# Kernel optimization log

Measured on AMD Instinct MI355X. Metric: run time of the kernel, lower is better.

## Reference

```python
import jax, jax.numpy as jnp
import numpy as np

OUT_H, OUT_W = 7, 7
SPATIAL_SCALE = 1.0


def setup_inputs() -> dict:
    key = jax.random.key(0)
    B, C, H, W = 4, 256, 64, 64
    N = 128
    features = jax.random.normal(key, (B, C, H, W), dtype=jnp.float32)
    rng = np.random.default_rng(0)
    bidx = rng.integers(0, B, N)
    x1 = rng.integers(0, W - 8, N)
    y1 = rng.integers(0, H - 8, N)
    x2 = np.minimum(x1 + rng.integers(4, 48, N), W - 1)
    y2 = np.minimum(y1 + rng.integers(4, 48, N), H - 1)
    rois = jnp.asarray(np.stack([bidx, x1, y1, x2, y2], axis=1), dtype=jnp.int32)
    return {"features": features, "rois": rois}


def _bin_bounds(n_bins, bin_sz, roi_sz):
    # h_start = int(h*bin_h); h_end = int((h+1)*bin_h); then clamp as in torch code
    bins = jnp.arange(n_bins)
    start = jnp.floor(bins[None, :] * bin_sz[:, None]).astype(jnp.int32)
    end = jnp.floor((bins[None, :] + 1) * bin_sz[:, None]).astype(jnp.int32)
    start = jnp.minimum(start, roi_sz[:, None] - 1)
    end = jnp.minimum(end, roi_sz[:, None])
    return start, end  # [N, n_bins]


def _roi_pool(features, rois):
    B, C, H, W = features.shape
    b = rois[:, 0]
    coords = (rois[:, 1:5].astype(jnp.float32) * SPATIAL_SCALE).astype(jnp.int32)
    x1, y1, x2, y2 = coords[:, 0], coords[:, 1], coords[:, 2], coords[:, 3]
    roi_h = y2 - y1 + 1  # inclusive slice y1:y2+1
    roi_w = x2 - x1 + 1
    bin_h = roi_h.astype(jnp.float32) / OUT_H
    bin_w = roi_w.astype(jnp.float32) / OUT_W

    hs, he = _bin_bounds(OUT_H, bin_h, roi_h)  # [N, OUT_H]
    ws, we = _bin_bounds(OUT_W, bin_w, roi_w)  # [N, OUT_W]
    valid = (he > hs)[:, :, None] & (we > ws)[:, None, :]  # [N, OUT_H, OUT_W]

    yy = jnp.arange(H)
    xx = jnp.arange(W)
    # absolute-coordinate bin masks (factorized along H and W)
    mask_h = (yy[None, None, :] >= (y1[:, None] + hs)[:, :, None]) & (
        yy[None, None, :] < (y1[:, None] + he)[:, :, None])  # [N, OUT_H, H]
    mask_w = (xx[None, None, :] >= (x1[:, None] + ws)[:, :, None]) & (
        xx[None, None, :] < (x1[:, None] + we)[:, :, None])  # [N, OUT_W, W]

    feat = features[b]  # [N, C, H, W] gather per ROI
    NEG = jnp.array(-jnp.inf, features.dtype)
    # reduce H per output row bin (OUT_H is small, fixed)
    rows = [jnp.where(mask_h[:, i, None, :, None], feat, NEG).max(axis=2)
            for i in range(OUT_H)]  # each [N, C, W]
    rowmax = jnp.stack(rows, axis=1)  # [N, OUT_H, C, W]
    cols = [jnp.where(mask_w[:, j, None, None, :], rowmax, NEG).max(axis=3)
            for j in range(OUT_W)]  # each [N, OUT_H, C]
    pooled = jnp.stack(cols, axis=3)  # [N, OUT_H, C, OUT_W]
    pooled = jnp.transpose(pooled, (0, 2, 1, 3))  # [N, C, OUT_H, OUT_W]
    # empty bins (h_end<=h_start or w_end<=w_start) stay zero, as in the torch code
    return jnp.where(valid[:, None, :, :], pooled, jnp.zeros((), features.dtype))


def reference(features, rois):
    return _roi_pool(features, rois)
```

## Files before the change

kernel.cpp:

```cpp
#include <hip/hip_runtime.h>
#include <math.h>

#define OUT_H 7
#define OUT_W 7
#define NBINS 49
#define PAD 66
#define TSZ (64 * PAD)

__global__ __launch_bounds__(256) void roipool_v18(
    const float* __restrict__ feat, const int* __restrict__ rois, int nroi,
    float* __restrict__ out)
{
    constexpr int C = 256, H = 64, W = 64, HW = H * W;
    __shared__ float tab[3 * TSZ];
    __shared__ unsigned char bh[128][8];
    __shared__ unsigned char bw[128][8];
    __shared__ unsigned char lst[128];
    __shared__ int cnt;

    const int bx = blockIdx.x;
    const int b  = bx >> 8;
    const int c  = bx & 255;
    const int t  = threadIdx.x;

    if (t == 0) cnt = 0;
    __syncthreads();

    const float* plane = feat + (size_t)(b * C + c) * HW;
#pragma unroll
    for (int i = 0; i < 4; ++i) {
        const int f = t + 256 * i;
        const float4 v = ((const float4*)plane)[f];
        const int row = f >> 4, c4 = f & 15;
        float* dst = &tab[row * PAD + c4 * 4];
        *(float2*)dst       = make_float2(v.x, v.y);
        *(float2*)(dst + 2) = make_float2(v.z, v.w);
    }

    {
        const int rr = t & 127;
        if (rr < nroi) {
            const int* rp = rois + rr * 5;
            if (t < 128) {
                const int y1 = rp[2];
                const int rh = rp[4] - y1 + 1;
#pragma unroll
                for (int k = 0; k <= 7; ++k)
                    bh[rr][k] = (unsigned char)(y1 + (k * rh) / OUT_H);
                if (rp[0] == b) {
                    const int p = atomicAdd(&cnt, 1);
                    lst[p] = (unsigned char)rr;
                }
            } else {
                const int x1 = rp[1];
                const int rw = rp[3] - x1 + 1;
#pragma unroll
                for (int k = 0; k <= 7; ++k)
                    bw[rr][k] = (unsigned char)(x1 + (k * rw) / OUT_W);
            }
        }
    }
    __syncthreads();

    const int row = t >> 2, q = t & 3, x0 = q * 16;
    float2 w2[8];
    {
        const float* src = &tab[row * PAD + x0];
        float2 r[8];
#pragma unroll
        for (int i = 0; i < 8; ++i) r[i] = ((const float2*)src)[i];
        const float nb = tab[row * PAD + (x0 + 16 < 64 ? x0 + 16 : 63)];
#pragma unroll
        for (int i = 0; i < 8; ++i) {
            const float nx = (i < 7) ? r[i + 1].x : nb;
            w2[i].x = fmaxf(r[i].x, r[i].y);
            w2[i].y = fmaxf(r[i].y, nx);
        }
        float* dst = &tab[TSZ + row * PAD + x0];
#pragma unroll
        for (int i = 0; i < 8; ++i) ((float2*)dst)[i] = w2[i];
    }
    __syncthreads();
    {
        const float2 nb2 =
            *(const float2*)&tab[TSZ + row * PAD + (x0 + 16 < 64 ? x0 + 16 : 62)];
        const float n16 = (x0 + 16 < 64) ? nb2.x : nb2.y;
        const float n17 = nb2.y;
        float2 u[8];
#pragma unroll
        for (int i = 0; i < 8; ++i) {
            const float d0 = (i < 7) ? w2[i + 1].x : n16;
            const float d1 = (i < 7) ? w2[i + 1].y : n17;
            u[i].x = fmaxf(w2[i].x, d0);
            u[i].y = fmaxf(w2[i].y, d1);
        }
        float* dst = &tab[2 * TSZ + row * PAD + x0];
#pragma unroll
        for (int i = 0; i < 8; ++i) ((float2*)dst)[i] = u[i];
    }
    __syncthreads();

    const int tot = cnt * NBINS;
    for (int g = t; g < tot; g += 256) {
        const int li  = g / NBINS;
        const int bin = g - li * NBINS;
        const int n   = lst[li];
        const int ph  = (bin * 37) >> 8;
        const int pw  = bin - ph * OUT_W;

        const int ys = bh[n][ph],  ye = bh[n][ph + 1];
        const int xs = bw[n][pw],  xe = bw[n][pw + 1];
        const int h = ye - ys, w = xe - xs;

        int toff, shf;
        if (w >= 4)      { toff = 2 * TSZ; shf = w - 4; }
        else if (w >= 2) { toff = TSZ;     shf = w - 2; }
        else             { toff = 0;       shf = 0;     }

        const int ylim = (h > 0) ? (ye - 1) : ys;
        float m = -INFINITY;
#pragma unroll
        for (int j = 0; j < 7; ++j) {
            int yj = ys + j;
            yj = yj < ylim ? yj : ylim;
            const int a = toff + yj * PAD + xs;
            m = fmaxf(m, fmaxf(tab[a], tab[a + shf]));
        }
        const float res = (h > 0 && w > 0) ? m : 0.0f;
        out[(n * C + c) * NBINS + bin] = res;
    }
}

extern "C" void kernel_launch(void* const* d_in, const int* in_sizes, int n_in,
                              void* d_out, int out_size, void* d_ws, size_t ws_size,
                              hipStream_t stream) {
    const float* feat = (const float*)d_in[0];
    const int*   rois = (const int*)d_in[1];
    float*       out  = (float*)d_out;

    int nroi = in_sizes[1] / 5;
    if (nroi > 128) nroi = 128;

    roipool_v18<<<4 * 256, 256, 0, stream>>>(feat, rois, nroi, out);
}
```

Baseline: 72.87 us.

## Drop width-2 max table, use lane shuffles and remove a barrier

Removes the width-2 horizontal-max shared table, cutting LDS from three feature-sized tables to two. Width-2 and width-3 bins now read the raw table, with an extra column pass for width 3. The width-4 table is built in the same phase by taking neighbour values through __shfl_down instead of a shared round-trip, which removes one __syncthreads and the initial barrier. It also batches the global float4 loads, defers the ROI-list atomics until after the table build, and adds a launch bound of 4 blocks. The goal is higher occupancy and less synchronisation, at the cost of more LDS reads for narrow bins.

Measured after the change: 72.51 us. No clear change (-0.5%).

```diff
diff --git a/kernel.cpp b/kernel.cpp
--- a/kernel.cpp
+++ b/kernel.cpp
@@ -7,12 +7,12 @@
 #define PAD 66
 #define TSZ (64 * PAD)
 
-__global__ __launch_bounds__(256) void roipool_v18(
+__global__ __launch_bounds__(256, 4) void roipool_v19(
     const float* __restrict__ feat, const int* __restrict__ rois, int nroi,
     float* __restrict__ out)
 {
     constexpr int C = 256, H = 64, W = 64, HW = H * W;
-    __shared__ float tab[3 * TSZ];
+    __shared__ float tab[2 * TSZ];
     __shared__ unsigned char bh[128][8];
     __shared__ unsigned char bw[128][8];
     __shared__ unsigned char lst[128];
@@ -24,79 +24,71 @@
     const int t  = threadIdx.x;
 
     if (t == 0) cnt = 0;
-    __syncthreads();
 
     const float* plane = feat + (size_t)(b * C + c) * HW;
+    float4 v[4];
+#pragma unroll
+    for (int i = 0; i < 4; ++i) v[i] = ((const float4*)plane)[t + 256 * i];
 #pragma unroll
     for (int i = 0; i < 4; ++i) {
         const int f = t + 256 * i;
-        const float4 v = ((const float4*)plane)[f];
         const int row = f >> 4, c4 = f & 15;
         float* dst = &tab[row * PAD + c4 * 4];
-        *(float2*)dst       = make_float2(v.x, v.y);
-        *(float2*)(dst + 2) = make_float2(v.z, v.w);
+        *(float2*)dst       = make_float2(v[i].x, v[i].y);
+        *(float2*)(dst + 2) = make_float2(v[i].z, v[i].w);
     }
 
-    {
-        const int rr = t & 127;
-        if (rr < nroi) {
-            const int* rp = rois + rr * 5;
-            if (t < 128) {
-                const int y1 = rp[2];
-                const int rh = rp[4] - y1 + 1;
+    bool mine = false;
+    const int rr = t & 127;
+    if (rr < nroi) {
+        const int* rp = rois + rr * 5;
+        if (t < 128) {
+            const int y1 = rp[2];
+            const int rh = rp[4] - y1 + 1;
 #pragma unroll
-                for (int k = 0; k <= 7; ++k)
-                    bh[rr][k] = (unsigned char)(y1 + (k * rh) / OUT_H);
-                if (rp[0] == b) {
-                    const int p = atomicAdd(&cnt, 1);
-                    lst[p] = (unsigned char)rr;
-                }
-            } else {
-                const int x1 = rp[1];
-                const int rw = rp[3] - x1 + 1;
+            for (int k = 0; k <= 7; ++k)
+                bh[rr][k] = (unsigned char)(y1 + (k * rh) / OUT_H);
+            mine = (rp[0] == b);
+        } else {
+            const int x1 = rp[1];
+            const int rw = rp[3] - x1 + 1;
 #pragma unroll
-                for (int k = 0; k <= 7; ++k)
-                    bw[rr][k] = (unsigned char)(x1 + (k * rw) / OUT_W);
-            }
+            for (int k = 0; k <= 7; ++k)
+                bw[rr][k] = (unsigned char)(x1 + (k * rw) / OUT_W);
         }
     }
     __syncthreads();
 
-    const int row = t >> 2, q = t & 3, x0 = q * 16;
-    float2 w2[8];
     {
+        const int row = t >> 2, q = t & 3, x0 = q * 16;
         const float* src = &tab[row * PAD + x0];
         float2 r[8];
 #pragma unroll
         for (int i = 0; i < 8; ++i) r[i] = ((const float2*)src)[i];
         const float nb = tab[row * PAD + (x0 + 16 < 64 ? x0 + 16 : 63)];
+        float2 w2[8];
 #pragma unroll
         for (int i = 0; i < 8; ++i) {
             const float nx = (i < 7) ? r[i + 1].x : nb;
             w2[i].x = fmaxf(r[i].x, r[i].y);
             w2[i].y = fmaxf(r[i].y, nx);
         }
+        const float n16 = __shfl_down(w2[0].x, 1);
+        const float n17 = __shfl_down(w2[0].y, 1);
         float* dst = &tab[TSZ + row * PAD + x0];
-#pragma unroll
-        for (int i = 0; i < 8; ++i) ((float2*)dst)[i] = w2[i];
-    }
-    __syncthreads();
-    {
-        const float2 nb2 =
-            *(const float2*)&tab[TSZ + row * PAD + (x0 + 16 < 64 ? x0 + 16 : 62)];
-        const float n16 = (x0 + 16 < 64) ? nb2.x : nb2.y;
-        const float n17 = nb2.y;
-        float2 u[8];
 #pragma unroll
         for (int i = 0; i < 8; ++i) {
             const float d0 = (i < 7) ? w2[i + 1].x : n16;
             const float d1 = (i < 7) ? w2[i + 1].y : n17;
-            u[i].x = fmaxf(w2[i].x, d0);
-            u[i].y = fmaxf(w2[i].y, d1);
+            float2 u;
+            u.x = fmaxf(w2[i].x, d0);
+            u.y = fmaxf(w2[i].y, d1);
+            ((float2*)dst)[i] = u;
         }
-        float* dst = &tab[2 * TSZ + row * PAD + x0];
-#pragma unroll
-        for (int i = 0; i < 8; ++i) ((float2*)dst)[i] = u[i];
+    }
+    if (mine) {
+        const int p = atomicAdd(&cnt, 1);
+        lst[p] = (unsigned char)rr;
     }
     __syncthreads();
 
@@ -112,10 +104,9 @@
         const int xs = bw[n][pw],  xe = bw[n][pw + 1];
         const int h = ye - ys, w = xe - xs;
 
-        int toff, shf;
-        if (w >= 4)      { toff = 2 * TSZ; shf = w - 4; }
-        else if (w >= 2) { toff = TSZ;     shf = w - 2; }
-        else             { toff = 0;       shf = 0;     }
+        const bool small = (w < 4);
+        const int toff = small ? 0 : TSZ;
+        const int s    = small ? (w > 1 ? w - 1 : 0) : (w - 4);
 
         const int ylim = (h > 0) ? (ye - 1) : ys;
         float m = -INFINITY;
@@ -124,7 +115,15 @@
             int yj = ys + j;
             yj = yj < ylim ? yj : ylim;
             const int a = toff + yj * PAD + xs;
-            m = fmaxf(m, fmaxf(tab[a], tab[a + shf]));
+            m = fmaxf(m, fmaxf(tab[a], tab[a + s]));
+        }
+        if (w == 3) {
+#pragma unroll
+            for (int j = 0; j < 7; ++j) {
+                int yj = ys + j;
+                yj = yj < ylim ? yj : ylim;
+                m = fmaxf(m, tab[yj * PAD + xs + 1]);
+            }
         }
         const float res = (h > 0 && w > 0) ? m : 0.0f;
         out[(n * C + c) * NBINS + bin] = res;
@@ -141,5 +140,5 @@
     int nroi = in_sizes[1] / 5;
     if (nroi > 128) nroi = 128;
 
-    roipool_v18<<<4 * 256, 256, 0, stream>>>(feat, rois, nroi, out);
+    roipool_v19<<<4 * 256, 256, 0, stream>>>(feat, rois, nroi, out);
 }
```
